# Kernel optimization log

Measured on AMD Instinct MI355X. Metric: run time of the kernel, lower is better.

The kernel has to match this reference:

```python
import jax, jax.numpy as jnp
import numpy as np
import math

EPS = 1e-6
MAX_NORM = 1.0 - 1e-3


def _clip_to_ball(x):
    # Keep point strictly inside the unit ball (||x|| < 1).
    norm = jnp.maximum(jnp.linalg.norm(x, axis=-1, keepdims=True), EPS)
    factor = jnp.minimum(MAX_NORM / norm, 1.0)
    return x * factor


def setup_inputs() -> dict:
    key = jax.random.key(0)
    k1, k2 = jax.random.split(key)
    B, C, D = 8192, 4096, 512
    euclidean_emb = jax.random.normal(k1, (B, D), dtype=jnp.float32)
    centroids = jax.random.uniform(k2, (C, D), dtype=jnp.float32, minval=-0.01, maxval=0.01)
    log_c = jnp.asarray(math.log(1.0), dtype=jnp.float32)
    return {"euclidean_emb": euclidean_emb, "log_c": log_c, "centroids": centroids}


def reference(euclidean_emb, log_c, centroids):
    # torch code used c = self.log_c.exp().item() -> c is detached scalar
    c = jax.lax.stop_gradient(jnp.exp(log_c))
    sqrt_c = jnp.sqrt(c)

    # expmap0: Euclidean -> Poincare ball
    v_norm = jnp.maximum(jnp.linalg.norm(euclidean_emb, axis=-1, keepdims=True), EPS)
    coeff = jnp.tanh(sqrt_c * v_norm) / (sqrt_c * v_norm)
    x_h = _clip_to_ball(coeff * euclidean_emb)   # (B, D)
    cen_h = _clip_to_ball(centroids)             # (C, D)

    # Pairwise Poincare distance via GEMM (same math as the expanded (B,C,D) form):
    # ||x - y||^2 = ||x||^2 + ||y||^2 - 2 <x, y>
    x2_raw = jnp.sum(x_h * x_h, axis=-1)         # (B,)
    y2_raw = jnp.sum(cen_h * cen_h, axis=-1)     # (C,)
    x2 = jnp.minimum(x2_raw, MAX_NORM ** 2)
    y2 = jnp.minimum(y2_raw, MAX_NORM ** 2)
    xy = x_h @ cen_h.T                           # (B, C) GEMM
    diff2 = x2_raw[:, None] + y2_raw[None, :] - 2.0 * xy

    denom = jnp.maximum((1.0 - c * x2)[:, None] * (1.0 - c * y2)[None, :], EPS)
    arg = jnp.maximum(1.0 + c * (2.0 * diff2) / denom, 1.0 + EPS)
    dists = jnp.arccosh(arg) / sqrt_c            # (B, C)
    return dists, x_h, cen_h
```

## Files before the change

### kernel.cpp

```cpp
#include <hip/hip_runtime.h>
#include <math.h>

#define EPSV 1e-6f
#define MAX_NORM (1.0f - 1e-3f)

typedef __attribute__((ext_vector_type(8))) short short8;
typedef __attribute__((ext_vector_type(4))) float f32x4;

__device__ inline ushort f32_to_bf16(float f) {
    union { float f; uint32_t u; } cv;
    cv.f = f;
    uint32_t u = cv.u;
    u += 0x7FFFu + ((u >> 16) & 1u);
    return (ushort)(u >> 16);
}

__device__ inline void glds16(const ushort* gsrc, ushort* ldsdst) {
    auto* g = (const __attribute__((address_space(1))) uint32_t*)gsrc;
    auto* l = (__attribute__((address_space(3))) uint32_t*)ldsdst;
    __builtin_amdgcn_global_load_lds(g, l, 16, 0, 0);
}

__device__ inline short8 ds_read128(const ushort* p) {
    auto* l3 = (const __attribute__((address_space(3))) ushort*)p;
    const uint32_t addr = (uint32_t)(uintptr_t)l3;
    short8 v;
    asm volatile("ds_read_b128 %0, %1" : "=&v"(v) : "v"(addr));
    return v;
}

__global__ void rows_emb_kernel(const float* __restrict__ emb,
                                const float* __restrict__ logc,
                                float* __restrict__ xh,
                                ushort* __restrict__ xbf,
                                float* __restrict__ x2raw,
                                float* __restrict__ dxv) {
    const int D = 512;
    const int row = blockIdx.x;
    const int lane = threadIdx.x;

    const float4* r4 = (const float4*)(emb + (size_t)row * D);
    float4 a = r4[2 * lane];
    float4 b = r4[2 * lane + 1];

    float ss = a.x * a.x + a.y * a.y + a.z * a.z + a.w * a.w
             + b.x * b.x + b.y * b.y + b.z * b.z + b.w * b.w;
#pragma unroll
    for (int off = 32; off > 0; off >>= 1) ss += __shfl_xor(ss, off, 64);

    const float c  = expf(logc[0]);
    const float sc = sqrtf(c);

    const float tn    = sqrtf(ss);
    const float vn    = fmaxf(tn, EPSV);
    const float coeff = tanhf(sc * vn) / (sc * vn);
    const float pre   = coeff * tn;
    const float fac   = fminf(MAX_NORM / fmaxf(pre, EPSV), 1.0f);
    const float scale = coeff * fac;

    float4 oa, ob;
    oa.x = a.x * scale; oa.y = a.y * scale; oa.z = a.z * scale; oa.w = a.w * scale;
    ob.x = b.x * scale; ob.y = b.y * scale; ob.z = b.z * scale; ob.w = b.w * scale;

    float4* o4 = (float4*)(xh + (size_t)row * D);
    o4[2 * lane]     = oa;
    o4[2 * lane + 1] = ob;

    union { ushort u[8]; uint4 v; } pk;
    pk.u[0] = f32_to_bf16(oa.x); pk.u[1] = f32_to_bf16(oa.y);
    pk.u[2] = f32_to_bf16(oa.z); pk.u[3] = f32_to_bf16(oa.w);
    pk.u[4] = f32_to_bf16(ob.x); pk.u[5] = f32_to_bf16(ob.y);
    pk.u[6] = f32_to_bf16(ob.z); pk.u[7] = f32_to_bf16(ob.w);
    ((uint4*)(xbf + (size_t)row * D))[lane] = pk.v;

    if (lane == 0) {
        const float sq = scale * scale * ss;
        x2raw[row] = sq;
        dxv[row]   = 1.0f - c * fminf(sq, MAX_NORM * MAX_NORM);
    }
}

__global__ void rows_cen_kernel(const float* __restrict__ cen,
                                const float* __restrict__ logc,
                                float* __restrict__ ch,
                                ushort* __restrict__ cbf,
                                float* __restrict__ y2raw,
                                float* __restrict__ dyv) {
    const int D = 512;
    const int row = blockIdx.x;
    const int lane = threadIdx.x;

    const float4* r4 = (const float4*)(cen + (size_t)row * D);
    float4 a = r4[2 * lane];
    float4 b = r4[2 * lane + 1];

    float ss = a.x * a.x + a.y * a.y + a.z * a.z + a.w * a.w
             + b.x * b.x + b.y * b.y + b.z * b.z + b.w * b.w;
#pragma unroll
    for (int off = 32; off > 0; off >>= 1) ss += __shfl_xor(ss, off, 64);

    const float c = expf(logc[0]);

    const float tn    = sqrtf(ss);
    const float scale = fminf(MAX_NORM / fmaxf(tn, EPSV), 1.0f);

    float4 oa, ob;
    oa.x = a.x * scale; oa.y = a.y * scale; oa.z = a.z * scale; oa.w = a.w * scale;
    ob.x = b.x * scale; ob.y = b.y * scale; ob.z = b.z * scale; ob.w = b.w * scale;

    float4* o4 = (float4*)(ch + (size_t)row * D);
    o4[2 * lane]     = oa;
    o4[2 * lane + 1] = ob;

    union { ushort u[8]; uint4 v; } pk;
    pk.u[0] = f32_to_bf16(oa.x); pk.u[1] = f32_to_bf16(oa.y);
    pk.u[2] = f32_to_bf16(oa.z); pk.u[3] = f32_to_bf16(oa.w);
    pk.u[4] = f32_to_bf16(ob.x); pk.u[5] = f32_to_bf16(ob.y);
    pk.u[6] = f32_to_bf16(ob.z); pk.u[7] = f32_to_bf16(ob.w);
    ((uint4*)(cbf + (size_t)row * D))[lane] = pk.v;

    if (lane == 0) {
        const float sq = scale * scale * ss;
        y2raw[row] = sq;
        dyv[row]   = 1.0f - c * fminf(sq, MAX_NORM * MAX_NORM);
    }
}

#define BM 256
#define BN 256
#define BKT 64
#define EPST 68
#define KDIM 512
#define NT 8
#define NCOLS 4096

__global__ __launch_bounds__(512, 2)
void gemm_epi_kernel(const ushort* __restrict__ Abf,
                     const ushort* __restrict__ Bbf,
                     const float* __restrict__ x2raw,
                     const float* __restrict__ dxv,
                     const float* __restrict__ y2raw,
                     const float* __restrict__ dyv,
                     const float* __restrict__ logc,
                     float* __restrict__ out) {
    __shared__ __align__(16) ushort ring[2][32768];

    const int tid  = threadIdx.x;
    const int lane = tid & 63;
    const int wid  = tid >> 6;
    const int wm   = wid >> 2;
    const int wn   = wid & 3;

    const int bm = blockIdx.y;
    const int bn = blockIdx.x;

    const ushort* Ab = Abf + (size_t)bm * BM * KDIM;
    const ushort* Bb = Bbf + (size_t)bn * BN * KDIM;

    f32x4 acc[8][4];
#pragma unroll
    for (int m = 0; m < 8; m++)
#pragma unroll
        for (int n = 0; n < 4; n++) acc[m][n] = (f32x4){0.f, 0.f, 0.f, 0.f};

    const size_t fragoff = (size_t)(lane & 15) * KDIM + ((lane >> 4) * 8);

    const ushort* gA0 = Ab + (size_t)(2 * wid * 16) * KDIM + fragoff;
    const ushort* gA1 = gA0 + 16 * KDIM;
    const ushort* gB0 = Bb + (size_t)(2 * wid * 16) * KDIM + fragoff;
    const ushort* gB1 = gB0 + 16 * KDIM;

    ushort* lA = &ring[0][0]     + wid * 2048;
    ushort* lB = &ring[0][16384] + wid * 2048;

    const ushort* rdA = &ring[0][0]     + wm * 8192 + lane * 8;
    const ushort* rdB = &ring[0][16384] + wn * 4096 + lane * 8;

    glds16(gA0,      lA);        glds16(gA0 + 32, lA + 512);
    glds16(gA1,      lA + 1024); glds16(gA1 + 32, lA + 1536);
    glds16(gB0,      lB);        glds16(gB0 + 32, lB + 512);
    glds16(gB1,      lB + 1024); glds16(gB1 + 32, lB + 1536);

    for (int t = 0; t < NT; ++t) {
        asm volatile("s_waitcnt vmcnt(0)" ::: "memory");
        __builtin_amdgcn_s_barrier();
        __builtin_amdgcn_sched_barrier(0);

        const int p32 = (t & 1) * 32768;
        const ushort* rA = rdA + p32;
        const ushort* rB = rdB + p32;

        const bool st = (t + 1 < NT);
        const int koff = (t + 1) * BKT;
        const int spd  = ((t + 1) & 1) * 32768;
        const ushort* sA0 = gA0 + koff;
        const ushort* sA1 = gA1 + koff;
        const ushort* sB0 = gB0 + koff;
        const ushort* sB1 = gB1 + koff;

        short8 bf[8], af[16];
#pragma unroll
        for (int n = 0; n < 4; n++) {
            bf[2 * n]     = ds_read128(rB + n * 1024);
            bf[2 * n + 1] = ds_read128(rB + n * 1024 + 512);
        }
        af[0] = ds_read128(rA);
        af[1] = ds_read128(rA + 512);
        af[2] = ds_read128(rA + 1024);
        af[3] = ds_read128(rA + 1536);

#pragma unroll
        for (int q = 0; q < 4; ++q) {
            if (st) {
                if (q == 0) { glds16(sA0, lA + spd);        glds16(sA0 + 32, lA + spd + 512); }
                if (q == 1) { glds16(sA1, lA + spd + 1024); glds16(sA1 + 32, lA + spd + 1536); }
                if (q == 2) { glds16(sB0, lB + spd);        glds16(sB0 + 32, lB + spd + 512); }
                if (q == 3) { glds16(sB1, lB + spd + 1024); glds16(sB1 + 32, lB + spd + 1536); }
            }
            if (q < 3) {
                af[4 * q + 4] = ds_read128(rA + (2 * q + 2) * 1024);
                af[4 * q + 5] = ds_read128(rA + (2 * q + 2) * 1024 + 512);
                af[4 * q + 6] = ds_read128(rA + (2 * q + 3) * 1024);
                af[4 * q + 7] = ds_read128(rA + (2 * q + 3) * 1024 + 512);
                asm volatile("s_waitcnt lgkmcnt(4)" ::: "memory");
            } else {
                asm volatile("s_waitcnt lgkmcnt(0)" ::: "memory");
            }
            __builtin_amdgcn_sched_barrier(0);
            __builtin_amdgcn_s_setprio(1);
#pragma unroll
            for (int kk = 0; kk < 2; kk++)
#pragma unroll
                for (int n = 0; n < 4; n++) {
                    acc[2 * q][n] = __builtin_amdgcn_mfma_f32_16x16x32_bf16(
                        af[4 * q + kk], bf[2 * n + kk], acc[2 * q][n], 0, 0, 0);
                    acc[2 * q + 1][n] = __builtin_amdgcn_mfma_f32_16x16x32_bf16(
                        af[4 * q + 2 + kk], bf[2 * n + kk], acc[2 * q + 1][n], 0, 0, 0);
                }
            __builtin_amdgcn_s_setprio(0);
        }
    }

    __syncthreads();

    const float c   = expf(logc[0]);
    const float rsc = 1.0f / sqrtf(c);
    const int l16 = lane & 15;
    const int lg  = lane >> 4;

    float* ep = (float*)((char*)&ring[0][0] + (size_t)wid * 4352);
    const int gr_base = bm * BM + wm * 128;
    const int gc_base = bn * BN + wn * 64;

#pragma unroll
    for (int m = 0; m < 8; m++) {
#pragma unroll
        for (int n = 0; n < 4; n++)
#pragma unroll
            for (int r = 0; r < 4; r++)
                ep[(lg * 4 + r) * EPST + n * 16 + l16] = acc[m][n][r];
        asm volatile("s_waitcnt lgkmcnt(0)" ::: "memory");

#pragma unroll
        for (int it = 0; it < 4; it++) {
            const int row = it * 4 + lg;
            const int gr  = gr_base + m * 16 + row;
            const int gc  = gc_base + l16 * 4;
            float4 xy4 = *(const float4*)&ep[row * EPST + l16 * 4];
            const float rx  = x2raw[gr];
            const float dxr = dxv[gr];
            const float4 ry4 = *(const float4*)&y2raw[gc];
            const float4 dy4 = *(const float4*)&dyv[gc];
            float4 o;
            {
                const float rden = __builtin_amdgcn_rcpf(fmaxf(dxr * dy4.x, EPSV));
                float t = fmaxf(2.0f * c * (rx + ry4.x - 2.0f * xy4.x) * rden, EPSV);
                o.x = __logf(1.0f + t + __builtin_amdgcn_sqrtf(t * (t + 2.0f))) * rsc;
            }
            {
                const float rden = __builtin_amdgcn_rcpf(fmaxf(dxr * dy4.y, EPSV));
                float t = fmaxf(2.0f * c * (rx + ry4.y - 2.0f * xy4.y) * rden, EPSV);
                o.y = __logf(1.0f + t + __builtin_amdgcn_sqrtf(t * (t + 2.0f))) * rsc;
            }
            {
                const float rden = __builtin_amdgcn_rcpf(fmaxf(dxr * dy4.z, EPSV));
                float t = fmaxf(2.0f * c * (rx + ry4.z - 2.0f * xy4.z) * rden, EPSV);
                o.z = __logf(1.0f + t + __builtin_amdgcn_sqrtf(t * (t + 2.0f))) * rsc;
            }
            {
                const float rden = __builtin_amdgcn_rcpf(fmaxf(dxr * dy4.w, EPSV));
                float t = fmaxf(2.0f * c * (rx + ry4.w - 2.0f * xy4.w) * rden, EPSV);
                o.w = __logf(1.0f + t + __builtin_amdgcn_sqrtf(t * (t + 2.0f))) * rsc;
            }
            *(float4*)&out[(size_t)gr * NCOLS + gc] = o;
        }
        asm volatile("s_waitcnt lgkmcnt(0)" ::: "memory");
    }
}

extern "C" void kernel_launch(void* const* d_in, const int* in_sizes, int n_in,
                              void* d_out, int out_size, void* d_ws, size_t ws_size,
                              hipStream_t stream) {
    const float* emb  = (const float*)d_in[0];
    const float* logc = (const float*)d_in[1];
    const float* cen  = (const float*)d_in[2];

    const int D = 512;
    const int B = in_sizes[0] / D;
    const int C = in_sizes[2] / D;

    float* out   = (float*)d_out;
    float* dists = out;
    float* xh    = out + (size_t)B * C;
    float* ch    = xh + (size_t)B * D;

    char* ws = (char*)d_ws;
    size_t off = 0;
    auto alloc = [&](size_t bytes) -> char* {
        char* p = ws + off;
        off += (bytes + 255) & ~(size_t)255;
        return p;
    };
    ushort* xbf   = (ushort*)alloc((size_t)B * D * sizeof(ushort));
    ushort* cbf   = (ushort*)alloc((size_t)C * D * sizeof(ushort));
    float*  x2raw = (float*)alloc((size_t)B * sizeof(float));
    float*  dxv   = (float*)alloc((size_t)B * sizeof(float));
    float*  y2raw = (float*)alloc((size_t)C * sizeof(float));
    float*  dyv   = (float*)alloc((size_t)C * sizeof(float));

    rows_emb_kernel<<<B, 64, 0, stream>>>(emb, logc, xh, xbf, x2raw, dxv);
    rows_cen_kernel<<<C, 64, 0, stream>>>(cen, logc, ch, cbf, y2raw, dyv);

    dim3 grid(C / BN, B / BM);
    gemm_epi_kernel<<<grid, 512, 0, stream>>>(xbf, cbf, x2raw, dxv, y2raw, dyv,
                                              logc, dists);
}
```

Measured before the change: 91.75 us.

## Switch GEMM mainloop to 3-stage ring with BK=32 and per-quarter barriers

```diff
diff --git a/kernel.cpp b/kernel.cpp
--- a/kernel.cpp
+++ b/kernel.cpp
@@ -128,13 +128,13 @@
 
 #define BM 256
 #define BN 256
-#define BKT 64
+#define BKT 32
 #define EPST 68
 #define KDIM 512
-#define NT 8
+#define NT 16
 #define NCOLS 4096
 
-__global__ __launch_bounds__(512, 2)
+__global__ __launch_bounds__(512, 1)
 void gemm_epi_kernel(const ushort* __restrict__ Abf,
                      const ushort* __restrict__ Bbf,
                      const float* __restrict__ x2raw,
@@ -143,7 +143,7 @@
                      const float* __restrict__ dyv,
                      const float* __restrict__ logc,
                      float* __restrict__ out) {
-    __shared__ __align__(16) ushort ring[2][32768];
+    __shared__ __align__(16) ushort ring[3 * 16384];
 
     const int tid  = threadIdx.x;
     const int lane = tid & 63;
@@ -165,79 +165,75 @@
 
     const size_t fragoff = (size_t)(lane & 15) * KDIM + ((lane >> 4) * 8);
 
-    const ushort* gA0 = Ab + (size_t)(2 * wid * 16) * KDIM + fragoff;
+    const ushort* gA0 = Ab + (size_t)(2 * wid) * 16 * KDIM + fragoff;
     const ushort* gA1 = gA0 + 16 * KDIM;
-    const ushort* gB0 = Bb + (size_t)(2 * wid * 16) * KDIM + fragoff;
+    const ushort* gB0 = Bb + (size_t)(2 * wid) * 16 * KDIM + fragoff;
     const ushort* gB1 = gB0 + 16 * KDIM;
 
-    ushort* lA = &ring[0][0]     + wid * 2048;
-    ushort* lB = &ring[0][16384] + wid * 2048;
-
-    const ushort* rdA = &ring[0][0]     + wm * 8192 + lane * 8;
-    const ushort* rdB = &ring[0][16384] + wn * 4096 + lane * 8;
-
-    glds16(gA0,      lA);        glds16(gA0 + 32, lA + 512);
-    glds16(gA1,      lA + 1024); glds16(gA1 + 32, lA + 1536);
-    glds16(gB0,      lB);        glds16(gB0 + 32, lB + 512);
-    glds16(gB1,      lB + 1024); glds16(gB1 + 32, lB + 1536);
+    ushort* lA = &ring[0]    + wid * 1024;
+    ushort* lB = &ring[8192] + wid * 1024;
+
+    const ushort* rdA = &ring[0]    + wm * 4096 + lane * 8;
+    const ushort* rdB = &ring[8192] + wn * 2048 + lane * 8;
+
+    auto stage_tile = [&](int r, int t) {
+        const int ko = t * BKT;
+        glds16(gA0 + ko, lA + r * 16384);
+        glds16(gA1 + ko, lA + r * 16384 + 512);
+        glds16(gB0 + ko, lB + r * 16384);
+        glds16(gB1 + ko, lB + r * 16384 + 512);
+    };
+
+    stage_tile(0, 0);
+    stage_tile(1, 1);
 
     for (int t = 0; t < NT; ++t) {
-        asm volatile("s_waitcnt vmcnt(0)" ::: "memory");
+        if (t < NT - 1) asm volatile("s_waitcnt vmcnt(4)" ::: "memory");
+        else            asm volatile("s_waitcnt vmcnt(0)" ::: "memory");
         __builtin_amdgcn_s_barrier();
-        __builtin_amdgcn_sched_barrier(0);
-
-        const int p32 = (t & 1) * 32768;
-        const ushort* rA = rdA + p32;
-        const ushort* rB = rdB + p32;
-
-        const bool st = (t + 1 < NT);
-        const int koff = (t + 1) * BKT;
-        const int spd  = ((t + 1) & 1) * 32768;
-        const ushort* sA0 = gA0 + koff;
-        const ushort* sA1 = gA1 + koff;
-        const ushort* sB0 = gB0 + koff;
-        const ushort* sB1 = gB1 + koff;
-
-        short8 bf[8], af[16];
-#pragma unroll
-        for (int n = 0; n < 4; n++) {
-            bf[2 * n]     = ds_read128(rB + n * 1024);
-            bf[2 * n + 1] = ds_read128(rB + n * 1024 + 512);
-        }
-        af[0] = ds_read128(rA);
-        af[1] = ds_read128(rA + 512);
-        af[2] = ds_read128(rA + 1024);
-        af[3] = ds_read128(rA + 1536);
+
+        const int r16 = (t % 3) * 16384;
+        const ushort* rA = rdA + r16;
+        const ushort* rB = rdB + r16;
+
+        const bool st  = (t + 2 < NT);
+        const int  sr  = ((t + 2) % 3) * 16384;
+        const int  sko = (t + 2) * BKT;
+
+        short8 bf[4];
 
 #pragma unroll
         for (int q = 0; q < 4; ++q) {
+            short8 a0, a1;
+            if (q == 0) {
+#pragma unroll
+                for (int n = 0; n < 4; n++)
+                    bf[n] = ds_read128(rB + n * 512);
+            }
+            a0 = ds_read128(rA + (2 * q) * 512);
+            a1 = ds_read128(rA + (2 * q + 1) * 512);
+
             if (st) {
-                if (q == 0) { glds16(sA0, lA + spd);        glds16(sA0 + 32, lA + spd + 512); }
-                if (q == 1) { glds16(sA1, lA + spd + 1024); glds16(sA1 + 32, lA + spd + 1536); }
-                if (q == 2) { glds16(sB0, lB + spd);        glds16(sB0 + 32, lB + spd + 512); }
-                if (q == 3) { glds16(sB1, lB + spd + 1024); glds16(sB1 + 32, lB + spd + 1536); }
-            }
-            if (q < 3) {
-                af[4 * q + 4] = ds_read128(rA + (2 * q + 2) * 1024);
-                af[4 * q + 5] = ds_read128(rA + (2 * q + 2) * 1024 + 512);
-                af[4 * q + 6] = ds_read128(rA + (2 * q + 3) * 1024);
-                af[4 * q + 7] = ds_read128(rA + (2 * q + 3) * 1024 + 512);
-                asm volatile("s_waitcnt lgkmcnt(4)" ::: "memory");
-            } else {
-                asm volatile("s_waitcnt lgkmcnt(0)" ::: "memory");
-            }
+                if (q == 0) glds16(gA0 + sko, lA + sr);
+                if (q == 1) glds16(gA1 + sko, lA + sr + 512);
+                if (q == 2) glds16(gB0 + sko, lB + sr);
+                if (q == 3) glds16(gB1 + sko, lB + sr + 512);
+            }
+
+            __builtin_amdgcn_s_barrier();
+            asm volatile("s_waitcnt lgkmcnt(0)" ::: "memory");
             __builtin_amdgcn_sched_barrier(0);
             __builtin_amdgcn_s_setprio(1);
 #pragma unroll
-            for (int kk = 0; kk < 2; kk++)
-#pragma unroll
-                for (int n = 0; n < 4; n++) {
-                    acc[2 * q][n] = __builtin_amdgcn_mfma_f32_16x16x32_bf16(
-                        af[4 * q + kk], bf[2 * n + kk], acc[2 * q][n], 0, 0, 0);
-                    acc[2 * q + 1][n] = __builtin_amdgcn_mfma_f32_16x16x32_bf16(
-                        af[4 * q + 2 + kk], bf[2 * n + kk], acc[2 * q + 1][n], 0, 0, 0);
-                }
+            for (int n = 0; n < 4; n++) {
+                acc[2 * q][n]     = __builtin_amdgcn_mfma_f32_16x16x32_bf16(
+                    a0, bf[n], acc[2 * q][n], 0, 0, 0);
+                acc[2 * q + 1][n] = __builtin_amdgcn_mfma_f32_16x16x32_bf16(
+                    a1, bf[n], acc[2 * q + 1][n], 0, 0, 0);
+            }
+            __builtin_amdgcn_sched_barrier(0);
             __builtin_amdgcn_s_setprio(0);
+            __builtin_amdgcn_s_barrier();
         }
     }
 
@@ -248,7 +244,7 @@
     const int l16 = lane & 15;
     const int lg  = lane >> 4;
 
-    float* ep = (float*)((char*)&ring[0][0] + (size_t)wid * 4352);
+    float* ep = (float*)((char*)&ring[0] + (size_t)wid * 4352);
     const int gr_base = bm * BM + wm * 128;
     const int gc_base = bn * BN + wn * 64;
 
```

Measured after the change: 85.67 us. -6.6%, faster.
